# Performance work log

Measured on AMD Instinct MI355X. Metric: run time of the kernel, lower is better.

The kernel has to match this reference:

```python
import jax, jax.numpy as jnp
import numpy as np

H, W = 5, 11          # fixed spatial map from ConvLSTM2D((5,11), ...)
P = H * W             # 55 pixels; 1x1 convs are per-pixel linear layers
HC = 64               # hidden channels
IC = 2                # input channels
FC_DIMS = [2 * HC * P, 3400, 1000, 500, 50]  # 7040 -> 3400 -> 1000 -> 500 -> 50


def setup_inputs() -> dict:
    key = jax.random.key(0)
    ks = jax.random.split(key, 24)
    B, T = 32, 256
    s = 0.05
    d = {}
    d["x1"] = jax.random.normal(ks[0], (B, T, IC, H, W), jnp.float32)
    d["x2"] = jax.random.normal(ks[1], (B, T, IC, H, W), jnp.float32)
    # ConvLSTM cell params: 1x1 convs fused into (in, 4*HC) matrices, gate order i,f,o,g
    d["wx1"] = jax.random.normal(ks[2], (IC, 4 * HC), jnp.float32) * s
    d["wh1"] = jax.random.normal(ks[3], (HC, 4 * HC), jnp.float32) * s
    d["bx1"] = jax.random.normal(ks[4], (4 * HC,), jnp.float32) * s
    d["bh1"] = jax.random.normal(ks[5], (4 * HC,), jnp.float32) * s
    d["wx2"] = jax.random.normal(ks[6], (IC, 4 * HC), jnp.float32) * s
    d["wh2"] = jax.random.normal(ks[7], (HC, 4 * HC), jnp.float32) * s
    d["bx2"] = jax.random.normal(ks[8], (4 * HC,), jnp.float32) * s
    d["bh2"] = jax.random.normal(ks[9], (4 * HC,), jnp.float32) * s
    # FC stack (stored as (in,out) so y = x @ W + b, equivalent to torch Linear)
    for i in range(4):
        fan_in, fan_out = FC_DIMS[i], FC_DIMS[i + 1]
        lim = 1.0 / np.sqrt(fan_in)
        d[f"fw{i+2}"] = jax.random.uniform(ks[10 + 2 * i], (fan_in, fan_out), jnp.float32, -lim, lim)
        d[f"fb{i+2}"] = jax.random.uniform(ks[11 + 2 * i], (fan_out,), jnp.float32, -lim, lim)
    return d


def _cell_step(h, c, gx, wh, bh):
    # gx: (B,P,4*HC) precomputed x contribution; h,c: (B,P,HC)
    g = gx + h @ wh + bh
    i, f, o, gg = jnp.split(g, 4, axis=-1)
    c = jax.nn.sigmoid(f) * c + jax.nn.sigmoid(i) * jnp.tanh(gg)
    h = jax.nn.sigmoid(o) * jnp.tanh(c)
    return h, c


def _sub_forward(x, wx1, wh1, bx1, bh1, wx2, wh2, bx2, bh2,
                 fw2, fb2, fw3, fb3, fw4, fb4, fw5, fb5):
    B, T = x.shape[0], x.shape[1]
    # (B,T,C,H,W) -> (B,T,P,C): pixels become a batch dim for the 1x1 convs
    xs = x.transpose(0, 1, 3, 4, 2).reshape(B, T, P, IC)
    # Precompute all input-to-gate projections once (big batched GEMM)
    gx1 = jnp.einsum('btpc,cd->btpd', xs, wx1) + bx1            # cell1: forward in time
    gx2 = jnp.einsum('btpc,cd->btpd', xs[:, ::-1], wx2) + bx2   # cell2: reversed in time
    h0 = jnp.zeros((B, P, HC), x.dtype)

    def step(carry, g):
        h1, c1, h2, c2 = carry
        g1, g2 = g
        h1, c1 = _cell_step(h1, c1, g1, wh1, bh1)
        h2, c2 = _cell_step(h2, c2, g2, wh2, bh2)
        return (h1, c1, h2, c2), None

    (h1, _, h2, _), _ = jax.lax.scan(
        step, (h0, h0, h0, h0),
        (gx1.transpose(1, 0, 2, 3), gx2.transpose(1, 0, 2, 3)))

    # torch.cat((h1,h2),1) on (B,HC,H,W) then flatten -> channel-major layout
    out = jnp.concatenate([h1.transpose(0, 2, 1), h2.transpose(0, 2, 1)], axis=1).reshape(B, -1)
    out = out @ fw2 + fb2
    out = out @ fw3 + fb3
    out = out @ fw4 + fb4
    out = out @ fw5 + fb5
    return out


def reference(x1, x2, wx1, wh1, bx1, bh1, wx2, wh2, bx2, bh2,
              fw2, fb2, fw3, fb3, fw4, fb4, fw5, fb5):
    args = (wx1, wh1, bx1, bh1, wx2, wh2, bx2, bh2,
            fw2, fb2, fw3, fb3, fw4, fb4, fw5, fb5)
    out1 = _sub_forward(x1, *args)
    out2 = _sub_forward(x2, *args)
    return (out1, out2)
```

## Files before the change

### kernel.cpp

```cpp
#include <hip/hip_runtime.h>


#define T_STEPS 256
#define PIX 55
#define MT 16
#define TILES 110
#define LOG2E 1.4426950408889634f
#define FC_SUB 64
#define FC_GRP 16

typedef float f32x4 __attribute__((ext_vector_type(4)));
typedef __bf16 bf16x8 __attribute__((ext_vector_type(8)));
typedef __bf16 bf16x4 __attribute__((ext_vector_type(4)));

__global__ __launch_bounds__(256) void lstm_kernel(
    const float* __restrict__ x1, const float* __restrict__ x2,
    const float* __restrict__ wx1, const float* __restrict__ wh1,
    const float* __restrict__ bx1, const float* __restrict__ bh1,
    const float* __restrict__ wx2, const float* __restrict__ wh2,
    const float* __restrict__ bx2, const float* __restrict__ bh2,
    float* __restrict__ feat)
{
    int bid  = blockIdx.x;
    int tile = bid % TILES;
    int cc   = bid / TILES;
    int sub  = cc >> 1, cell = cc & 1;
    const float* x  = sub  ? x2  : x1;
    const float* wx = cell ? wx2 : wx1;
    const float* wh = cell ? wh2 : wh1;
    const float* bx = cell ? bx2 : bx1;
    const float* bh = cell ? bh2 : bh1;

    int tid  = threadIdx.x;
    int w    = tid >> 6;
    int l    = tid & 63;
    int quad = l >> 4;
    int c16  = l & 15;

    __shared__ float xl[MT * 514];
    __shared__ __align__(16) __bf16 hb[2][2][MT][72];

    {
        int seq0 = tile * MT;
        for (int i = 0; i < 32; ++i) {
            int idx = tid + 256 * i;
            int m = idx >> 9;
            int tc = idx & 511;
            int t = tc >> 1, c = tc & 1;
            int seq = seq0 + m;
            int b = seq / PIX, p = seq % PIX;
            xl[m * 514 + tc] = x[((b * T_STEPS + t) * 2 + c) * PIX + p];
        }
    }
    {
        __bf16* hz = &hb[0][0][0][0];
        for (int i = tid; i < 2 * 2 * MT * 72; i += 256) hz[i] = (__bf16)0.0f;
    }

    bf16x8 Whi[4][2], Wlo[4][2];
    float btot[4][4], wxa[4][4], wxb[4][4];
#pragma unroll
    for (int g = 0; g < 4; ++g) {
        int col = 64 * g + 16 * w + c16;
#pragma unroll
        for (int r = 0; r < 4; ++r) {
            int u = 64 * g + 16 * w + 4 * quad + r;
            btot[g][r] = bx[u] + bh[u];
            wxa[g][r]  = wx[u];
            wxb[g][r]  = wx[256 + u];
        }
#pragma unroll
        for (int q = 0; q < 2; ++q) {
#pragma unroll
            for (int j = 0; j < 8; ++j) {
                int k = 32 * q + 8 * quad + j;
                float wv = wh[k * 256 + col];
                __bf16 hi = (__bf16)wv;
                Whi[g][q][j] = hi;
                Wlo[g][q][j] = (__bf16)(wv - (float)hi);
            }
        }
    }

    float cst[4]  = {0.f, 0.f, 0.f, 0.f};
    float hfin[4] = {0.f, 0.f, 0.f, 0.f};

    __syncthreads();
    float2 xv = *(const float2*)&xl[c16 * 514 + (cell ? (T_STEPS - 1) : 0) * 2];

#pragma unroll 2
    for (int t = 0; t < T_STEPS; ++t) {
        int rb = t & 1, wb = rb ^ 1;

        bf16x8 Bh[2], Bl[2];
#pragma unroll
        for (int q = 0; q < 2; ++q) {
            Bh[q] = *(const bf16x8*)&hb[rb][0][c16][32 * q + 8 * quad];
            Bl[q] = *(const bf16x8*)&hb[rb][1][c16][32 * q + 8 * quad];
        }

        f32x4 acc[4];
#pragma unroll
        for (int g = 0; g < 4; ++g) {
#pragma unroll
            for (int r = 0; r < 4; ++r)
                acc[g][r] = fmaf(xv.y, wxb[g][r], fmaf(xv.x, wxa[g][r], btot[g][r]));
        }
#pragma unroll
        for (int g = 0; g < 4; ++g)
            acc[g] = __builtin_amdgcn_mfma_f32_16x16x32_bf16(Whi[g][0], Bh[0], acc[g], 0, 0, 0);
#pragma unroll
        for (int g = 0; g < 4; ++g)
            acc[g] = __builtin_amdgcn_mfma_f32_16x16x32_bf16(Whi[g][1], Bh[1], acc[g], 0, 0, 0);
#pragma unroll
        for (int g = 0; g < 4; ++g)
            acc[g] = __builtin_amdgcn_mfma_f32_16x16x32_bf16(Wlo[g][0], Bh[0], acc[g], 0, 0, 0);
#pragma unroll
        for (int g = 0; g < 4; ++g)
            acc[g] = __builtin_amdgcn_mfma_f32_16x16x32_bf16(Wlo[g][1], Bh[1], acc[g], 0, 0, 0);
#pragma unroll
        for (int g = 0; g < 4; ++g)
            acc[g] = __builtin_amdgcn_mfma_f32_16x16x32_bf16(Whi[g][0], Bl[0], acc[g], 0, 0, 0);
#pragma unroll
        for (int g = 0; g < 4; ++g)
            acc[g] = __builtin_amdgcn_mfma_f32_16x16x32_bf16(Whi[g][1], Bl[1], acc[g], 0, 0, 0);

        float ei[4], ef[4], eo[4], eg[4];
#pragma unroll
        for (int r = 0; r < 4; ++r) {
            ei[r] = __builtin_amdgcn_exp2f(-LOG2E * acc[0][r]);
            ef[r] = __builtin_amdgcn_exp2f(-LOG2E * acc[1][r]);
            eo[r] = __builtin_amdgcn_exp2f(-LOG2E * acc[2][r]);
            eg[r] = __builtin_amdgcn_exp2f(-2.0f * LOG2E * acc[3][r]);
        }

        bf16x4 ph, pl;
#pragma unroll
        for (int r = 0; r < 4; ++r) {
            float sf  = __builtin_amdgcn_rcpf(1.0f + ef[r]);
            float itg = (1.0f - eg[r]) * __builtin_amdgcn_rcpf((1.0f + ei[r]) * (1.0f + eg[r]));
            float c   = fmaf(sf, cst[r], itg);
            cst[r] = c;
            float ec = __builtin_amdgcn_exp2f(-2.0f * LOG2E * c);
            float h  = (1.0f - ec) * __builtin_amdgcn_rcpf((1.0f + eo[r]) * (1.0f + ec));
            hfin[r] = h;
            __bf16 hi = (__bf16)h;
            ph[r] = hi;
            pl[r] = (__bf16)(h - (float)hi);
        }
        *(bf16x4*)&hb[wb][0][c16][16 * w + 4 * quad] = ph;
        *(bf16x4*)&hb[wb][1][c16][16 * w + 4 * quad] = pl;

        {
            int txn = (cell ? (T_STEPS - 2 - t) : (t + 1)) & 255;
            xv = *(const float2*)&xl[c16 * 514 + txn * 2];
        }
        __syncthreads();
    }

    {
        int seq = tile * MT + c16;
        int b = seq / PIX, p = seq % PIX;
#pragma unroll
        for (int r = 0; r < 4; ++r) {
            int u = 16 * w + 4 * quad + r;
            feat[(size_t)(sub * 32 + b) * 7040 + (cell * 64 + u) * PIX + p] = hfin[r];
        }
    }
}

__global__ __launch_bounds__(256) void fc_init(
    const float* __restrict__ b2, const float* __restrict__ b3,
    const float* __restrict__ b4, const float* __restrict__ b5,
    float* __restrict__ t1, float* __restrict__ t2,
    float* __restrict__ t3, float* __restrict__ o)
{
    int i = blockIdx.x * 256 + threadIdx.x;
    const int n1 = 64 * 3400, n2 = 64 * 1000, n3 = 64 * 500, n4 = 64 * 50;
    if (i < n1) { t1[i] = b2[i % 3400]; return; }
    i -= n1;
    if (i < n2) { t2[i] = b3[i % 1000]; return; }
    i -= n2;
    if (i < n3) { t3[i] = b4[i % 500]; return; }
    i -= n3;
    if (i < n4) { o[i] = b5[i % 50]; }
}

__global__ __launch_bounds__(256) void fc_gemm(const float* __restrict__ A,
                                               const float* __restrict__ W,
                                               float* __restrict__ out,
                                               int K, int N, int kchunk) {
    __shared__ __align__(16) float al[FC_SUB * 68];
    int tid = threadIdx.x;
    int l   = tid & 63;
    int wv  = tid >> 6;
    int k0   = blockIdx.y * kchunk;
    int kend = min(K, k0 + kchunk);

    int n  = blockIdx.x * 64 + l;
    int ne = min(n, N - 1);

    float acc[16];
#pragma unroll
    for (int i = 0; i < 16; ++i) acc[i] = 0.0f;

    for (int ks = k0; ks < kend; ks += FC_SUB) {
        int kcur = min(FC_SUB, kend - ks);
        __syncthreads();
        if (kcur == FC_SUB) {
#pragma unroll
            for (int i = 0; i < 16; ++i) {
                int idx = tid + 256 * i;
                int m = idx >> 6, kc = idx & 63;
                al[kc * 68 + m] = A[(size_t)m * K + ks + kc];
            }
        } else {
#pragma unroll
            for (int i = 0; i < 16; ++i) {
                int idx = tid + 256 * i;
                int m = idx >> 6, kc = idx & 63;
                if (kc < kcur) al[kc * 68 + m] = A[(size_t)m * K + ks + kc];
            }
        }
        __syncthreads();

        const float* wr = W + (size_t)ks * N + ne;
        if (kcur == FC_SUB) {
#pragma unroll
            for (int g8 = 0; g8 < FC_SUB / FC_GRP; ++g8) {
                float wbuf[FC_GRP];
#pragma unroll
                for (int j = 0; j < FC_GRP; ++j)
                    wbuf[j] = wr[(size_t)(g8 * FC_GRP + j) * N];
#pragma unroll
                for (int j = 0; j < FC_GRP; ++j) {
                    const float4* ap = (const float4*)&al[(g8 * FC_GRP + j) * 68 + 16 * wv];
#pragma unroll
                    for (int i = 0; i < 4; ++i) {
                        float4 a = ap[i];
                        acc[4 * i + 0] = fmaf(a.x, wbuf[j], acc[4 * i + 0]);
                        acc[4 * i + 1] = fmaf(a.y, wbuf[j], acc[4 * i + 1]);
                        acc[4 * i + 2] = fmaf(a.z, wbuf[j], acc[4 * i + 2]);
                        acc[4 * i + 3] = fmaf(a.w, wbuf[j], acc[4 * i + 3]);
                    }
                }
            }
        } else {
            int kc0 = 0;
            for (; kc0 + FC_GRP <= kcur; kc0 += FC_GRP) {
                float wbuf[FC_GRP];
#pragma unroll
                for (int j = 0; j < FC_GRP; ++j)
                    wbuf[j] = wr[(size_t)(kc0 + j) * N];
#pragma unroll
                for (int j = 0; j < FC_GRP; ++j) {
                    const float4* ap = (const float4*)&al[(kc0 + j) * 68 + 16 * wv];
#pragma unroll
                    for (int i = 0; i < 4; ++i) {
                        float4 a = ap[i];
                        acc[4 * i + 0] = fmaf(a.x, wbuf[j], acc[4 * i + 0]);
                        acc[4 * i + 1] = fmaf(a.y, wbuf[j], acc[4 * i + 1]);
                        acc[4 * i + 2] = fmaf(a.z, wbuf[j], acc[4 * i + 2]);
                        acc[4 * i + 3] = fmaf(a.w, wbuf[j], acc[4 * i + 3]);
                    }
                }
            }
            for (; kc0 < kcur; ++kc0) {
                float wvv = wr[(size_t)kc0 * N];
                const float4* ap = (const float4*)&al[kc0 * 68 + 16 * wv];
#pragma unroll
                for (int i = 0; i < 4; ++i) {
                    float4 a = ap[i];
                    acc[4 * i + 0] = fmaf(a.x, wvv, acc[4 * i + 0]);
                    acc[4 * i + 1] = fmaf(a.y, wvv, acc[4 * i + 1]);
                    acc[4 * i + 2] = fmaf(a.z, wvv, acc[4 * i + 2]);
                    acc[4 * i + 3] = fmaf(a.w, wvv, acc[4 * i + 3]);
                }
            }
        }
    }

    if (n < N) {
        float* pr = out + n;
#pragma unroll
        for (int i = 0; i < 16; ++i)
            unsafeAtomicAdd(&pr[(size_t)(16 * wv + i) * N], acc[i]);
    }
}

extern "C" void kernel_launch(void* const* d_in, const int* in_sizes, int n_in,
                              void* d_out, int out_size, void* d_ws, size_t ws_size,
                              hipStream_t stream) {
    const float* x1  = (const float*)d_in[0];
    const float* x2  = (const float*)d_in[1];
    const float* wx1 = (const float*)d_in[2];
    const float* wh1 = (const float*)d_in[3];
    const float* bx1 = (const float*)d_in[4];
    const float* bh1 = (const float*)d_in[5];
    const float* wx2 = (const float*)d_in[6];
    const float* wh2 = (const float*)d_in[7];
    const float* bx2 = (const float*)d_in[8];
    const float* bh2 = (const float*)d_in[9];
    const float* fw2 = (const float*)d_in[10];
    const float* fb2 = (const float*)d_in[11];
    const float* fw3 = (const float*)d_in[12];
    const float* fb3 = (const float*)d_in[13];
    const float* fw4 = (const float*)d_in[14];
    const float* fb4 = (const float*)d_in[15];
    const float* fw5 = (const float*)d_in[16];
    const float* fb5 = (const float*)d_in[17];

    char* ws = (char*)d_ws;
    float* feat = (float*)ws;
    float* t1   = feat + (size_t)64 * 7040;
    float* t2   = t1   + (size_t)64 * 3400;
    float* t3   = t2   + (size_t)64 * 1000;
    float* o    = (float*)d_out;

    fc_init<<<dim3(1238), dim3(256), 0, stream>>>(fb2, fb3, fb4, fb5, t1, t2, t3, o);

    lstm_kernel<<<dim3(440), dim3(256), 0, stream>>>(
        x1, x2, wx1, wh1, bx1, bh1, wx2, wh2, bx2, bh2, feat);

    fc_gemm<<<dim3(54, 28), dim3(256), 0, stream>>>(feat, fw2, t1, 7040, 3400, 256);
    fc_gemm<<<dim3(16, 54), dim3(256), 0, stream>>>(t1, fw3, t2, 3400, 1000, 64);
    fc_gemm<<<dim3(8, 16), dim3(256), 0, stream>>>(t2, fw4, t3, 1000, 500, 64);
    fc_gemm<<<dim3(1, 16), dim3(256), 0, stream>>>(t3, fw5, o, 500, 50, 32);
}
```

Baseline: 565.7 us.

## Drop LDS staging in FC GEMM, read activations via wave-uniform scalar loads

The FC GEMM no longer stages activation tiles in shared memory with block barriers. Each wave now reads its 16 activation rows straight from global memory at a wave-uniform address (readfirstlane), which lets the compiler use scalar loads. K-splits are also made finer so more blocks run in parallel. The aim is to remove barrier and LDS overhead from these bandwidth-bound layers, at the cost of more atomic adds and more scalar-cache traffic.

```diff
diff --git a/kernel.cpp b/kernel.cpp
--- a/kernel.cpp
+++ b/kernel.cpp
@@ -6,7 +6,6 @@
 #define MT 16
 #define TILES 110
 #define LOG2E 1.4426950408889634f
-#define FC_SUB 64
 #define FC_GRP 16
 
 typedef float f32x4 __attribute__((ext_vector_type(4)));
@@ -190,101 +189,47 @@
                                                const float* __restrict__ W,
                                                float* __restrict__ out,
                                                int K, int N, int kchunk) {
-    __shared__ __align__(16) float al[FC_SUB * 68];
-    int tid = threadIdx.x;
-    int l   = tid & 63;
-    int wv  = tid >> 6;
+    int tid  = threadIdx.x;
+    int l    = tid & 63;
+    int row0 = __builtin_amdgcn_readfirstlane((tid >> 6) * 16);
     int k0   = blockIdx.y * kchunk;
     int kend = min(K, k0 + kchunk);
 
     int n  = blockIdx.x * 64 + l;
     int ne = min(n, N - 1);
 
+    const float* ar = A + (size_t)row0 * K;
+    const float* wp = W + ne;
+
     float acc[16];
 #pragma unroll
     for (int i = 0; i < 16; ++i) acc[i] = 0.0f;
 
-    for (int ks = k0; ks < kend; ks += FC_SUB) {
-        int kcur = min(FC_SUB, kend - ks);
-        __syncthreads();
-        if (kcur == FC_SUB) {
-#pragma unroll
-            for (int i = 0; i < 16; ++i) {
-                int idx = tid + 256 * i;
-                int m = idx >> 6, kc = idx & 63;
-                al[kc * 68 + m] = A[(size_t)m * K + ks + kc];
-            }
-        } else {
-#pragma unroll
-            for (int i = 0; i < 16; ++i) {
-                int idx = tid + 256 * i;
-                int m = idx >> 6, kc = idx & 63;
-                if (kc < kcur) al[kc * 68 + m] = A[(size_t)m * K + ks + kc];
-            }
-        }
-        __syncthreads();
-
-        const float* wr = W + (size_t)ks * N + ne;
-        if (kcur == FC_SUB) {
-#pragma unroll
-            for (int g8 = 0; g8 < FC_SUB / FC_GRP; ++g8) {
-                float wbuf[FC_GRP];
-#pragma unroll
-                for (int j = 0; j < FC_GRP; ++j)
-                    wbuf[j] = wr[(size_t)(g8 * FC_GRP + j) * N];
-#pragma unroll
-                for (int j = 0; j < FC_GRP; ++j) {
-                    const float4* ap = (const float4*)&al[(g8 * FC_GRP + j) * 68 + 16 * wv];
-#pragma unroll
-                    for (int i = 0; i < 4; ++i) {
-                        float4 a = ap[i];
-                        acc[4 * i + 0] = fmaf(a.x, wbuf[j], acc[4 * i + 0]);
-                        acc[4 * i + 1] = fmaf(a.y, wbuf[j], acc[4 * i + 1]);
-                        acc[4 * i + 2] = fmaf(a.z, wbuf[j], acc[4 * i + 2]);
-                        acc[4 * i + 3] = fmaf(a.w, wbuf[j], acc[4 * i + 3]);
-                    }
-                }
-            }
-        } else {
-            int kc0 = 0;
-            for (; kc0 + FC_GRP <= kcur; kc0 += FC_GRP) {
-                float wbuf[FC_GRP];
-#pragma unroll
-                for (int j = 0; j < FC_GRP; ++j)
-                    wbuf[j] = wr[(size_t)(kc0 + j) * N];
-#pragma unroll
-                for (int j = 0; j < FC_GRP; ++j) {
-                    const float4* ap = (const float4*)&al[(kc0 + j) * 68 + 16 * wv];
-#pragma unroll
-                    for (int i = 0; i < 4; ++i) {
-                        float4 a = ap[i];
-                        acc[4 * i + 0] = fmaf(a.x, wbuf[j], acc[4 * i + 0]);
-                        acc[4 * i + 1] = fmaf(a.y, wbuf[j], acc[4 * i + 1]);
-                        acc[4 * i + 2] = fmaf(a.z, wbuf[j], acc[4 * i + 2]);
-                        acc[4 * i + 3] = fmaf(a.w, wbuf[j], acc[4 * i + 3]);
-                    }
-                }
-            }
-            for (; kc0 < kcur; ++kc0) {
-                float wvv = wr[(size_t)kc0 * N];
-                const float4* ap = (const float4*)&al[kc0 * 68 + 16 * wv];
-#pragma unroll
-                for (int i = 0; i < 4; ++i) {
-                    float4 a = ap[i];
-                    acc[4 * i + 0] = fmaf(a.x, wvv, acc[4 * i + 0]);
-                    acc[4 * i + 1] = fmaf(a.y, wvv, acc[4 * i + 1]);
-                    acc[4 * i + 2] = fmaf(a.z, wvv, acc[4 * i + 2]);
-                    acc[4 * i + 3] = fmaf(a.w, wvv, acc[4 * i + 3]);
-                }
-            }
-        }
+    int ks = k0;
+    for (; ks + FC_GRP <= kend; ks += FC_GRP) {
+        float wbuf[FC_GRP];
+#pragma unroll
+        for (int j = 0; j < FC_GRP; ++j)
+            wbuf[j] = wp[(size_t)(ks + j) * N];
+#pragma unroll
+        for (int j = 0; j < FC_GRP; ++j) {
+#pragma unroll
+            for (int m = 0; m < 16; ++m)
+                acc[m] = fmaf(ar[(size_t)m * K + ks + j], wbuf[j], acc[m]);
+        }
+    }
+    for (; ks < kend; ++ks) {
+        float wvv = wp[(size_t)ks * N];
+#pragma unroll
+        for (int m = 0; m < 16; ++m)
+            acc[m] = fmaf(ar[(size_t)m * K + ks], wvv, acc[m]);
     }
 
     if (n < N) {
         float* pr = out + n;
 #pragma unroll
         for (int i = 0; i < 16; ++i)
-            unsafeAtomicAdd(&pr[(size_t)(16 * wv + i) * N], acc[i]);
+            unsafeAtomicAdd(&pr[(size_t)(row0 + i) * N], acc[i]);
     }
 }
 
@@ -322,8 +267,8 @@
     lstm_kernel<<<dim3(440), dim3(256), 0, stream>>>(
         x1, x2, wx1, wh1, bx1, bh1, wx2, wh2, bx2, bh2, feat);
 
-    fc_gemm<<<dim3(54, 28), dim3(256), 0, stream>>>(feat, fw2, t1, 7040, 3400, 256);
-    fc_gemm<<<dim3(16, 54), dim3(256), 0, stream>>>(t1, fw3, t2, 3400, 1000, 64);
-    fc_gemm<<<dim3(8, 16), dim3(256), 0, stream>>>(t2, fw4, t3, 1000, 500, 64);
-    fc_gemm<<<dim3(1, 16), dim3(256), 0, stream>>>(t3, fw5, o, 500, 50, 32);
-}
+    fc_gemm<<<dim3(54, 44), dim3(256), 0, stream>>>(feat, fw2, t1, 7040, 3400, 160);
+    fc_gemm<<<dim3(16, 107), dim3(256), 0, stream>>>(t1, fw3, t2, 3400, 1000, 32);
+    fc_gemm<<<dim3(8, 63), dim3(256), 0, stream>>>(t2, fw4, t3, 1000, 500, 16);
+    fc_gemm<<<dim3(1, 32), dim3(256), 0, stream>>>(t3, fw5, o, 500, 50, 16);
+}
```

New measurement: 632.8 us. 11.8% more time.
